# Kernel optimization log

Hardware: AMD Instinct MI355X
Metric: run time of the kernel (lower is better)

## Reference

```python
import math
import jax, jax.numpy as jnp
import numpy as np

B, N, C = 16, 2048, 128
ETA, TAU = 1.0, 1.5


def setup_inputs() -> dict:
    key = jax.random.key(0)
    k1, k2, k3, k4, k5 = jax.random.split(key, 5)
    H_t = jax.random.normal(k1, (B, N, C), dtype=jnp.float32)
    A_stat = jax.random.uniform(k2, (N, N), dtype=jnp.float32)
    M_mask = jax.random.uniform(k3, (N, N), dtype=jnp.float32)
    # nn.Linear(d_model, d_model, bias=False) weights, shape [out, in]
    scale = 1.0 / math.sqrt(C)
    Wq = jax.random.uniform(k4, (C, C), dtype=jnp.float32, minval=-scale, maxval=scale)
    Wk = jax.random.uniform(k5, (C, C), dtype=jnp.float32, minval=-scale, maxval=scale)
    return {"H_t": H_t, "A_stat": A_stat, "M_mask": M_mask, "Wq": Wq, "Wk": Wk}


def reference(H_t, A_stat, M_mask, Wq, Wk):
    c = H_t.shape[-1]
    neg_inf = jnp.array(-jnp.inf, dtype=H_t.dtype)
    # Linear: x @ W.T
    Q = jnp.einsum('bnc,dc->bnd', H_t, Wq)
    K = jnp.einsum('bnc,dc->bnd', H_t, Wk)
    # scaled QK^T, temperature
    logits = jnp.einsum('bnd,bmd->bnm', Q, K) / (math.sqrt(c) * TAU)
    # symmetrize
    logits = 0.5 * (logits + jnp.swapaxes(logits, -1, -2))
    # diagonal mask
    n = logits.shape[-1]
    eye = jnp.eye(n, dtype=bool)
    logits = jnp.where(eye[None, :, :], neg_inf, logits)
    # static-adjacency bias with zeroed diagonal
    A_bias = jnp.where(eye, 0.0, A_stat)
    logits = logits + ETA * A_bias[None, :, :]
    # external mask
    logits = jnp.where((M_mask <= 0)[None, :, :], neg_inf, logits)
    return jax.nn.softmax(logits, axis=-1)
```

## Files before the change

### kernel.cpp

```cpp
#include <hip/hip_runtime.h>
#include <hip/hip_bf16.h>
#include <hip/hip_fp16.h>
#include <math.h>

#define Bn 16
#define Nn 2048
#define Cn 128

typedef __attribute__((ext_vector_type(8))) short bf16x8;
typedef __attribute__((ext_vector_type(4))) float f32x4;

constexpr float SCALE = 0.029462782549439476f;
constexpr float SHIFT = 4.0f;

#define LDS_STRIDE 136

__device__ __forceinline__ const bf16x8* as_frag(const __hip_bfloat16* p){
    return reinterpret_cast<const bf16x8*>(p);
}

__global__ __launch_bounds__(256) void transpose_w_kernel(
    const float* __restrict__ Wq, const float* __restrict__ Wk,
    float* __restrict__ WqT, float* __restrict__ WkT)
{
    int idx = blockIdx.x * 256 + threadIdx.x;
    int d = idx >> 7, c = idx & 127;
    WqT[c*Cn + d] = Wq[idx];
    WkT[c*Cn + d] = Wk[idx];
}

__global__ __launch_bounds__(256) void prep_bias_kernel(
    const float* __restrict__ A, const float* __restrict__ M, __half* __restrict__ CB)
{
    size_t idx = (size_t)blockIdx.x * 256 + threadIdx.x;
    int n = (int)(idx >> 11), m = (int)(idx & (Nn-1));
    float a = A[idx];
    float mm = M[idx];
    float v = (mm <= 0.0f || n == m) ? -INFINITY : a;
    CB[idx] = __float2half(v);
}

__global__ __launch_bounds__(256) void qk_kernel(
    const float* __restrict__ H, const float* __restrict__ WqT, const float* __restrict__ WkT,
    __hip_bfloat16* __restrict__ Qb, __hip_bfloat16* __restrict__ Kb)
{
    __shared__ __align__(16) float Hs[32*Cn];
    const int t = threadIdx.x;
    const size_t row0 = (size_t)blockIdx.x * 32;
    const float4* src = reinterpret_cast<const float4*>(H + row0*Cn);
    float4* dst = reinterpret_cast<float4*>(Hs);
    #pragma unroll
    for (int i = 0; i < 4; i++) dst[i*256 + t] = src[i*256 + t];
    __syncthreads();
    const int d = t & 127, rh = t >> 7;
    float accq[16], acck[16];
    #pragma unroll
    for (int r = 0; r < 16; r++){ accq[r] = 0.f; acck[r] = 0.f; }
    for (int cb = 0; cb < Cn; cb += 4){
        float wq[4], wk[4];
        #pragma unroll
        for (int j = 0; j < 4; j++){ wq[j] = WqT[(cb+j)*Cn + d]; wk[j] = WkT[(cb+j)*Cn + d]; }
        #pragma unroll
        for (int r = 0; r < 16; r++){
            float4 h = *reinterpret_cast<const float4*>(&Hs[(rh*16+r)*Cn + cb]);
            accq[r] += h.x*wq[0] + h.y*wq[1] + h.z*wq[2] + h.w*wq[3];
            acck[r] += h.x*wk[0] + h.y*wk[1] + h.z*wk[2] + h.w*wk[3];
        }
    }
    #pragma unroll
    for (int r = 0; r < 16; r++){
        size_t row = row0 + rh*16 + r;
        Qb[row*Cn + d] = __float2bfloat16(accq[r]);
        Kb[row*Cn + d] = __float2bfloat16(acck[r]);
    }
}

template<int PASS>
__global__ __launch_bounds__(256) void attn_kernel(
    const __hip_bfloat16* __restrict__ Qb, const __hip_bfloat16* __restrict__ Kb,
    const __half* __restrict__ CB, float* __restrict__ rowsum, float* __restrict__ out)
{
    __shared__ __align__(16) __hip_bfloat16 Ks_s[64*LDS_STRIDE];
    __shared__ __align__(16) __hip_bfloat16 Qs_s[64*LDS_STRIDE];
    const int t = threadIdx.x;
    const int wave = t >> 6, lane = t & 63;
    const int q = lane >> 4, lc = lane & 15;
    const int batch = blockIdx.y;
    const int n0 = blockIdx.x * 64;
    const size_t rbase = (size_t)batch * Nn;

    const int nA = n0 + wave*16 + lc;
    bf16x8 aQ[4], aK[4];
    #pragma unroll
    for (int ks = 0; ks < 4; ks++){
        aQ[ks] = *as_frag(Qb + (rbase + nA)*Cn + ks*32 + q*8);
        aK[ks] = *as_frag(Kb + (rbase + nA)*Cn + ks*32 + q*8);
    }

    int nout[4];
    #pragma unroll
    for (int r = 0; r < 4; r++) nout[r] = n0 + wave*16 + q*4 + r;

    float sumacc[4] = {0.f,0.f,0.f,0.f};
    float rs_inv[4];
    if (PASS == 1){
        #pragma unroll
        for (int r = 0; r < 4; r++) rs_inv[r] = 1.0f / rowsum[rbase + nout[r]];
    }

    for (int mc = 0; mc < Nn/64; mc++){
        __syncthreads();
        {
            const int4* gK = reinterpret_cast<const int4*>(Kb + (rbase + (size_t)mc*64)*Cn);
            const int4* gQ = reinterpret_cast<const int4*>(Qb + (rbase + (size_t)mc*64)*Cn);
            #pragma unroll
            for (int i = 0; i < 4; i++){
                int id = i*256 + t;
                int r = id >> 4, c2 = id & 15;
                int4 vk = gK[id];
                int4 vq = gQ[id];
                *reinterpret_cast<int4*>(&Ks_s[r*LDS_STRIDE + c2*8]) = vk;
                *reinterpret_cast<int4*>(&Qs_s[r*LDS_STRIDE + c2*8]) = vq;
            }
        }
        __syncthreads();
        #pragma unroll
        for (int mt = 0; mt < 4; mt++){
            const int m0 = mc*64 + mt*16;
            bf16x8 bK[4], bQ[4];
            #pragma unroll
            for (int ks = 0; ks < 4; ks++){
                bK[ks] = *as_frag(&Ks_s[(mt*16+lc)*LDS_STRIDE + ks*32 + q*8]);
                bQ[ks] = *as_frag(&Qs_s[(mt*16+lc)*LDS_STRIDE + ks*32 + q*8]);
            }
            f32x4 acc = {0.f,0.f,0.f,0.f};
            #pragma unroll
            for (int ks = 0; ks < 4; ks++){
                acc = __builtin_amdgcn_mfma_f32_16x16x32_bf16(aQ[ks], bK[ks], acc, 0, 0, 0);
                acc = __builtin_amdgcn_mfma_f32_16x16x32_bf16(aK[ks], bQ[ks], acc, 0, 0, 0);
            }
            const int m = m0 + lc;
            #pragma unroll
            for (int r = 0; r < 4; r++){
                const int n = nout[r];
                float logit = fmaf(acc[r], SCALE, __half2float(CB[(size_t)n*Nn + m]));
                float e = __expf(logit - SHIFT);
                if (PASS == 0) sumacc[r] += e;
                else out[(rbase + n)*Nn + m] = e * rs_inv[r];
            }
        }
    }
    if (PASS == 0){
        #pragma unroll
        for (int r = 0; r < 4; r++){
            float s = sumacc[r];
            s += __shfl_xor(s, 1);
            s += __shfl_xor(s, 2);
            s += __shfl_xor(s, 4);
            s += __shfl_xor(s, 8);
            if (lc == 0) rowsum[rbase + nout[r]] = s;
        }
    }
}

extern "C" void kernel_launch(void* const* d_in, const int* in_sizes, int n_in,
                              void* d_out, int out_size, void* d_ws, size_t ws_size,
                              hipStream_t stream)
{
    const float* H  = (const float*)d_in[0];
    const float* A  = (const float*)d_in[1];
    const float* M  = (const float*)d_in[2];
    const float* Wq = (const float*)d_in[3];
    const float* Wk = (const float*)d_in[4];
    float* out = (float*)d_out;
    char* ws = (char*)d_ws;
    __hip_bfloat16* Qb = (__hip_bfloat16*)(ws + 0);
    __hip_bfloat16* Kb = (__hip_bfloat16*)(ws + 8388608);
    float* rowsum      = (float*)(ws + 16777216);
    float* WqT         = (float*)(ws + 16908288);
    float* WkT         = (float*)(ws + 16973824);
    __half* CB         = (__half*)(ws + 17039360);

    transpose_w_kernel<<<64, 256, 0, stream>>>(Wq, Wk, WqT, WkT);
    prep_bias_kernel<<<(Nn*Nn)/256, 256, 0, stream>>>(A, M, CB);
    qk_kernel<<<(Bn*Nn)/32, 256, 0, stream>>>(H, WqT, WkT, Qb, Kb);
    attn_kernel<0><<<dim3(Nn/64, Bn), 256, 0, stream>>>(Qb, Kb, CB, rowsum, out);
    attn_kernel<1><<<dim3(Nn/64, Bn), 256, 0, stream>>>(Qb, Kb, CB, rowsum, out);
}
```

Measured before the change: 459.0 us.

## Replace two-pass attention recompute with single exp pass plus normalization kernel

The second attention pass, which recomputed QK^T, bias and exp only to scale by the row sum, is replaced. The single attention kernel now writes unnormalized exponentials and the inverse row sum, and a streaming norm kernel rescales the output in place. The weight-transpose kernel is also merged into the bias prep kernel to save a launch. This trades a full MFMA and bias-read recompute for an extra read and write of the 256MB output.

```diff
diff --git a/kernel.cpp b/kernel.cpp
--- a/kernel.cpp
+++ b/kernel.cpp
@@ -19,18 +19,10 @@
     return reinterpret_cast<const bf16x8*>(p);
 }
 
-__global__ __launch_bounds__(256) void transpose_w_kernel(
+__global__ __launch_bounds__(256) void prep_kernel(
+    const float* __restrict__ A, const float* __restrict__ M, __half* __restrict__ CB,
     const float* __restrict__ Wq, const float* __restrict__ Wk,
     float* __restrict__ WqT, float* __restrict__ WkT)
-{
-    int idx = blockIdx.x * 256 + threadIdx.x;
-    int d = idx >> 7, c = idx & 127;
-    WqT[c*Cn + d] = Wq[idx];
-    WkT[c*Cn + d] = Wk[idx];
-}
-
-__global__ __launch_bounds__(256) void prep_bias_kernel(
-    const float* __restrict__ A, const float* __restrict__ M, __half* __restrict__ CB)
 {
     size_t idx = (size_t)blockIdx.x * 256 + threadIdx.x;
     int n = (int)(idx >> 11), m = (int)(idx & (Nn-1));
@@ -38,6 +30,12 @@
     float mm = M[idx];
     float v = (mm <= 0.0f || n == m) ? -INFINITY : a;
     CB[idx] = __float2half(v);
+    if (blockIdx.x < 64) {
+        int widx = (int)idx;
+        int d = widx >> 7, c = widx & 127;
+        WqT[c*Cn + d] = Wq[widx];
+        WkT[c*Cn + d] = Wk[widx];
+    }
 }
 
 __global__ __launch_bounds__(256) void qk_kernel(
@@ -75,8 +73,7 @@
     }
 }
 
-template<int PASS>
-__global__ __launch_bounds__(256) void attn_kernel(
+__global__ __launch_bounds__(256) void attn_e_kernel(
     const __hip_bfloat16* __restrict__ Qb, const __hip_bfloat16* __restrict__ Kb,
     const __half* __restrict__ CB, float* __restrict__ rowsum, float* __restrict__ out)
 {
@@ -102,11 +99,6 @@
     for (int r = 0; r < 4; r++) nout[r] = n0 + wave*16 + q*4 + r;
 
     float sumacc[4] = {0.f,0.f,0.f,0.f};
-    float rs_inv[4];
-    if (PASS == 1){
-        #pragma unroll
-        for (int r = 0; r < 4; r++) rs_inv[r] = 1.0f / rowsum[rbase + nout[r]];
-    }
 
     for (int mc = 0; mc < Nn/64; mc++){
         __syncthreads();
@@ -145,21 +137,35 @@
                 const int n = nout[r];
                 float logit = fmaf(acc[r], SCALE, __half2float(CB[(size_t)n*Nn + m]));
                 float e = __expf(logit - SHIFT);
-                if (PASS == 0) sumacc[r] += e;
-                else out[(rbase + n)*Nn + m] = e * rs_inv[r];
+                sumacc[r] += e;
+                out[(rbase + n)*Nn + m] = e;
             }
         }
     }
-    if (PASS == 0){
-        #pragma unroll
-        for (int r = 0; r < 4; r++){
-            float s = sumacc[r];
-            s += __shfl_xor(s, 1);
-            s += __shfl_xor(s, 2);
-            s += __shfl_xor(s, 4);
-            s += __shfl_xor(s, 8);
-            if (lc == 0) rowsum[rbase + nout[r]] = s;
-        }
+    #pragma unroll
+    for (int r = 0; r < 4; r++){
+        float s = sumacc[r];
+        s += __shfl_xor(s, 1);
+        s += __shfl_xor(s, 2);
+        s += __shfl_xor(s, 4);
+        s += __shfl_xor(s, 8);
+        if (lc == 0) rowsum[rbase + nout[r]] = 1.0f / s;
+    }
+}
+
+__global__ __launch_bounds__(256) void norm_kernel(
+    float* __restrict__ out, const float* __restrict__ rsinv)
+{
+    const size_t t0 = (size_t)blockIdx.x * 256 + threadIdx.x;
+    const size_t stride = (size_t)4096 * 256;
+    float4* o4 = reinterpret_cast<float4*>(out);
+    #pragma unroll
+    for (int i = 0; i < 16; i++){
+        size_t idx = t0 + (size_t)i * stride;
+        float4 v = o4[idx];
+        float r = rsinv[idx >> 9];
+        v.x *= r; v.y *= r; v.z *= r; v.w *= r;
+        o4[idx] = v;
     }
 }
 
@@ -181,9 +187,8 @@
     float* WkT         = (float*)(ws + 16973824);
     __half* CB         = (__half*)(ws + 17039360);
 
-    transpose_w_kernel<<<64, 256, 0, stream>>>(Wq, Wk, WqT, WkT);
-    prep_bias_kernel<<<(Nn*Nn)/256, 256, 0, stream>>>(A, M, CB);
+    prep_kernel<<<(Nn*Nn)/256, 256, 0, stream>>>(A, M, CB, Wq, Wk, WqT, WkT);
     qk_kernel<<<(Bn*Nn)/32, 256, 0, stream>>>(H, WqT, WkT, Qb, Kb);
-    attn_kernel<0><<<dim3(Nn/64, Bn), 256, 0, stream>>>(Qb, Kb, CB, rowsum, out);
-    attn_kernel<1><<<dim3(Nn/64, Bn), 256, 0, stream>>>(Qb, Kb, CB, rowsum, out);
+    attn_e_kernel<<<dim3(Nn/64, Bn), 256, 0, stream>>>(Qb, Kb, CB, rowsum, out);
+    norm_kernel<<<4096, 256, 0, stream>>>(out, rowsum);
 }
```

New measurement: 510.9 us. 11.3% more time.
